# Kernel tuning notes

Measured on AMD Instinct MI355X. Metric: run time of the kernel, lower is better.

## Reference

```python
import jax, jax.numpy as jnp
import numpy as np

B, T, X, H, Z = 64, 2048, 128, 256, 64


def setup_inputs() -> dict:
    key = jax.random.key(0)
    ks = jax.random.split(key, 6)
    s = lambda n: 1.0 / np.sqrt(n).astype(np.float32)
    return {
        "x_seq": jax.random.normal(ks[0], (B, T, X), jnp.float32),
        # LSTMCell params packed as [i|f|g|o] gates. Flax: input dense has no bias,
        # hidden dense has bias.
        "Wi": jax.random.normal(ks[1], (X, 4 * H), jnp.float32) * s(X),
        "Wh": jax.random.normal(ks[2], (H, 4 * H), jnp.float32) * s(H),
        "bh": jnp.zeros((4 * H,), jnp.float32),
        # head: Dense(H) -> relu -> Dense(2Z)
        "W1": jax.random.normal(ks[3], (H, H), jnp.float32) * s(H),
        "b1": jnp.zeros((H,), jnp.float32),
        "W2": jax.random.normal(ks[4], (H, 2 * Z), jnp.float32) * s(H),
        "b2": jnp.zeros((2 * Z,), jnp.float32),
    }


def _forward(x_seq, Wi, Wh, bh, W1, b1, W2, b2):
    Bsz = x_seq.shape[0]
    Hd = Wh.shape[0]
    # Precompute input projection for all timesteps (one big GEMM).
    x_proj = jnp.einsum('btx,xg->btg', x_seq, Wi)  # (B, T, 4H)
    xp = jnp.swapaxes(x_proj, 0, 1)  # (T, B, 4H) for scan

    def step(carry, xp_t):
        c, h = carry
        gates = xp_t + h @ Wh + bh  # (B, 4H)
        i, f, g, o = jnp.split(gates, 4, axis=-1)
        i = jax.nn.sigmoid(i)
        f = jax.nn.sigmoid(f)
        g = jnp.tanh(g)
        o = jax.nn.sigmoid(o)
        c = f * c + i * g
        h = o * jnp.tanh(c)
        hid = jax.nn.relu(h @ W1 + b1)
        out = hid @ W2 + b2  # (B, 2Z)
        return (c, h), out

    c0 = jnp.zeros((Bsz, Hd), x_seq.dtype)
    h0 = jnp.zeros((Bsz, Hd), x_seq.dtype)
    _, outs = jax.lax.scan(step, (c0, h0), xp)  # outs: (T, B, 2Z)
    outs = jnp.swapaxes(outs, 0, 1)  # (B, T, 2Z)
    mu_seq, log_sigma_seq = jnp.split(outs, 2, axis=-1)
    return mu_seq, log_sigma_seq


def reference(x_seq, Wi, Wh, bh, W1, b1, W2, b2):
    return _forward(x_seq, Wi, Wh, bh, W1, b1, W2, b2)
```

## Files before the change

### kernel.cpp

```cpp
#include <hip/hip_runtime.h>

typedef _Float16 f16;
typedef _Float16 h2 __attribute__((ext_vector_type(2)));
typedef _Float16 h8 __attribute__((ext_vector_type(8)));
typedef float f4 __attribute__((ext_vector_type(4)));

constexpr int Bb = 64, Tt = 2048, Xx = 128, Hh = 256, G4 = 1024, Z2 = 128;

__device__ __forceinline__ float fdot2f(h2 a, h2 b, float c) {
#if __has_builtin(__builtin_amdgcn_fdot2)
  return __builtin_amdgcn_fdot2(a, b, c, false);
#else
  return c + (float)a[0] * (float)b[0] + (float)a[1] * (float)b[1];
#endif
}
__device__ __forceinline__ float tanhf_(float x) {
  float e = __expf(2.0f * x);
  return 1.0f - 2.0f * __builtin_amdgcn_rcpf(e + 1.0f);
}
__device__ __forceinline__ h2 bch2(unsigned int u) { return __builtin_bit_cast(h2, u); }

template <int CTRL>
__device__ __forceinline__ float qb(float v) {
  return __builtin_bit_cast(float,
      __builtin_amdgcn_mov_dpp(__builtin_bit_cast(int, v), CTRL, 0xf, 0xf, true));
}

__global__ void cast_f16_k(const float* __restrict__ in, f16* __restrict__ out, int n) {
  int i = (blockIdx.x * 256 + threadIdx.x) * 4;
  if (i >= n) return;
  float4 v = *(const float4*)(in + i);
  h2 a = {(f16)v.x, (f16)v.y};
  h2 b = {(f16)v.z, (f16)v.w};
  uint2 o = {__builtin_bit_cast(unsigned int, a), __builtin_bit_cast(unsigned int, b)};
  *(uint2*)(out + i) = o;
}

__global__ void cast_whT_k(const float* __restrict__ Wh, f16* __restrict__ WhT) {
  int idx = blockIdx.x * 256 + threadIdx.x;
  int r = idx >> 8, k = idx & 255;
  int gcol = ((r & 3) << 8) | (r >> 2);
  WhT[idx] = (f16)Wh[(long)k * G4 + gcol];
}

__global__ __launch_bounds__(256, 4) void gemm_f16_k(
    const f16* __restrict__ A, const f16* __restrict__ Bm, const float* __restrict__ bias,
    f16* __restrict__ C16, float* __restrict__ Cmu, float* __restrict__ Cls,
    int N, int K, int a_shift, int a_ostride, int a_t0,
    int mode, int o_t0, int tcshift)
{
  __shared__ __align__(16) f16 At[64][48];
  __shared__ __align__(16) f16 Bt[64][48];
  const int tid = threadIdx.x;
  const int mblk = blockIdx.x, nblk = blockIdx.y;
  const int w = tid >> 6, lane = tid & 63;

  const int sa_row = tid >> 2, sa_k = (tid & 3) * 8;
  const int m_g = mblk * 64 + sa_row;
  const long arow = (long)(m_g >> a_shift) * a_ostride + a_t0 + (m_g & ((1 << a_shift) - 1));
  const f16* aptr = A + arow * K + sa_k;
  const int sb_k = tid >> 3, sb_n = (tid & 7) * 8;
  const f16* bptr = Bm + (long)sb_k * N + nblk * 64 + sb_n;

  f4 acc[4];
#pragma unroll
  for (int i = 0; i < 4; ++i) acc[i] = (f4){0.f, 0.f, 0.f, 0.f};

  const int arow_l = w * 16 + (lane & 15);
  const int k0 = (lane >> 4) * 8;

  for (int kk = 0; kk < K; kk += 32) {
    uint4 av = *(const uint4*)(aptr + kk);
    uint4 bv = *(const uint4*)(bptr + (long)kk * N);
    __syncthreads();
    *(uint4*)&At[sa_row][sa_k] = av;
    h8 bx = __builtin_bit_cast(h8, bv);
#pragma unroll
    for (int j = 0; j < 8; ++j) Bt[sb_n + j][sb_k] = bx[j];
    __syncthreads();
    h8 af = *(const h8*)&At[arow_l][k0];
#pragma unroll
    for (int nt = 0; nt < 4; ++nt) {
      h8 bf = *(const h8*)&Bt[nt * 16 + (lane & 15)][k0];
      acc[nt] = __builtin_amdgcn_mfma_f32_16x16x32_f16(af, bf, acc[nt], 0, 0, 0);
    }
  }

  const int row_l = w * 16 + ((lane >> 4) << 2);
  const int col_l = lane & 15;
#pragma unroll
  for (int nt = 0; nt < 4; ++nt) {
    int gcol = nblk * 64 + nt * 16 + col_l;
    float bv = bias[gcol];
#pragma unroll
    for (int r = 0; r < 4; ++r) {
      int gm = mblk * 64 + row_l + r;
      float val = acc[nt][r] + bv;
      if (mode == 1) val = fmaxf(val, 0.f);
      if (mode <= 1) {
        C16[(long)gm * N + gcol] = (f16)val;
      } else {
        int bb = gm >> tcshift, tl = gm & ((1 << tcshift) - 1);
        long orow = (long)bb * Tt + o_t0 + tl;
        if (gcol < 64) Cmu[orow * 64 + gcol] = val;
        else Cls[orow * 64 + (gcol - 64)] = val;
      }
    }
  }
}

__global__ void __launch_bounds__(1024) __attribute__((amdgpu_waves_per_eu(4, 4)))
lstm_rec_k(
    const f16* __restrict__ WhT, const f16* __restrict__ xp,
    f16* __restrict__ hout, float* __restrict__ c_state, f16* __restrict__ h_state,
    int TC, int first)
{
  const int b = blockIdx.x, tid = threadIdx.x;
  const int j = tid >> 2, g = tid & 3;
  __shared__ __align__(16) h2 hbuf[2][128];
  __shared__ __align__(16) h2 wlds[9][1024][4];

  h2 w[92];
  {
    const uint4* p4 = (const uint4*)(WhT + (long)tid * Hh);
#pragma unroll
    for (int i = 0; i < 23; ++i) {
      uint4 v = p4[i];
      w[4 * i + 0] = bch2(v.x); w[4 * i + 1] = bch2(v.y);
      w[4 * i + 2] = bch2(v.z); w[4 * i + 3] = bch2(v.w);
    }
#pragma unroll
    for (int gg = 0; gg < 9; ++gg) *(uint4*)&wlds[gg][tid][0] = p4[23 + gg];
  }

  float c = first ? 0.f : c_state[b * Hh + j];
  if (tid < 128) {
    h2 hz = {(f16)0.f, (f16)0.f};
    hbuf[0][tid] = first ? hz : ((const h2*)h_state)[b * 128 + tid];
  }
  __syncthreads();

  const float sgn = (g == 2) ? 2.0f : -1.0f;
  const int xcol = (g << 8) | j;
  const f16* xptr = xp + (long)b * TC * G4 + xcol;
  const f16* xend = xptr + (long)(TC - 1) * G4;
  f16 xc = *xptr;
  int p = 0;
  for (int t = 0; t < TC; ++t) {
    const f16* xnp = (xptr == xend) ? xptr : xptr + G4;
    f16 xn = *xnp;

    float a0 = (float)xc, a1 = 0.f;
    const uint4* hb4 = (const uint4*)&hbuf[p][0];
#pragma unroll
    for (int i = 0; i < 23; ++i) {
      uint4 hv = hb4[i];
      a0 = fdot2f(w[4 * i + 0], bch2(hv.x), a0);
      a1 = fdot2f(w[4 * i + 1], bch2(hv.y), a1);
      a0 = fdot2f(w[4 * i + 2], bch2(hv.z), a0);
      a1 = fdot2f(w[4 * i + 3], bch2(hv.w), a1);
    }
#pragma unroll
    for (int gg = 0; gg < 9; ++gg) {
      uint4 hv = hb4[23 + gg];
      uint4 wv = *(const uint4*)&wlds[gg][tid][0];
      a0 = fdot2f(bch2(wv.x), bch2(hv.x), a0);
      a1 = fdot2f(bch2(wv.y), bch2(hv.y), a1);
      a0 = fdot2f(bch2(wv.z), bch2(hv.z), a0);
      a1 = fdot2f(bch2(wv.w), bch2(hv.w), a1);
    }
    float a = a0 + a1;

    float e = __expf(sgn * a);
    float r = __builtin_amdgcn_rcpf(1.0f + e);
    float act = (g == 2) ? 1.0f - 2.0f * r : r;

    float ai = qb<0x00>(act), af = qb<0x55>(act);
    float ag = qb<0xAA>(act), ao = qb<0xFF>(act);
    c = af * c + ai * ag;
    float hval = ao * tanhf_(c);
    if (g == 3) {
      f16 hh = (f16)hval;
      ((f16*)&hbuf[p ^ 1][0])[j] = hh;
      hout[((long)b * TC + t) * Hh + j] = hh;
    }
    __syncthreads();
    p ^= 1;
    xc = xn;
    xptr = xnp;
  }
  if (g == 0) c_state[b * Hh + j] = c;
  if (tid < 128) ((h2*)h_state)[b * 128 + tid] = hbuf[p][tid];
}

extern "C" void kernel_launch(void* const* d_in, const int* in_sizes, int n_in,
                              void* d_out, int out_size, void* d_ws, size_t ws_size,
                              hipStream_t stream)
{
  const float* x  = (const float*)d_in[0];
  const float* Wi = (const float*)d_in[1];
  const float* Wh = (const float*)d_in[2];
  const float* bh = (const float*)d_in[3];
  const float* W1 = (const float*)d_in[4];
  const float* b1 = (const float*)d_in[5];
  const float* W2 = (const float*)d_in[6];
  const float* b2 = (const float*)d_in[7];
  float* out = (float*)d_out;

  char* ws = (char*)d_ws;
  size_t off = 0;
  auto alloc = [&](size_t bytes) -> char* {
    char* p = ws + off;
    off = (off + bytes + 255) & ~(size_t)255;
    return p;
  };
  f16* x16   = (f16*)alloc((size_t)Bb * Tt * Xx * 2);
  f16* wi16  = (f16*)alloc((size_t)Xx * G4 * 2);
  f16* whT16 = (f16*)alloc((size_t)G4 * Hh * 2);
  f16* w116  = (f16*)alloc((size_t)Hh * Hh * 2);
  f16* w216  = (f16*)alloc((size_t)Hh * Z2 * 2);
  float* cst = (float*)alloc((size_t)Bb * Hh * 4);
  f16* hst   = (f16*)alloc((size_t)Bb * Hh * 2);

  int tc = 2048;
  while (tc > 32) {
    size_t need = (size_t)Bb * tc * G4 * 2 + (size_t)Bb * tc * Hh * 2;
    if (off + need <= ws_size) break;
    tc >>= 1;
  }
  int tcsh = __builtin_ctz((unsigned)tc);
  f16* xp16 = (f16*)alloc((size_t)Bb * tc * G4 * 2);
  f16* h16  = (f16*)alloc((size_t)Bb * tc * Hh * 2);
  f16* hid16 = xp16;

  cast_f16_k<<<(Bb * Tt * Xx) / 1024, 256, 0, stream>>>(x, x16, Bb * Tt * Xx);
  cast_f16_k<<<(Xx * G4) / 1024, 256, 0, stream>>>(Wi, wi16, Xx * G4);
  cast_f16_k<<<(Hh * Hh) / 1024, 256, 0, stream>>>(W1, w116, Hh * Hh);
  cast_f16_k<<<(Hh * Z2) / 1024, 256, 0, stream>>>(W2, w216, Hh * Z2);
  cast_whT_k<<<(Hh * G4) / 256, 256, 0, stream>>>(Wh, whT16);

  float* mu = out;
  float* ls = out + (size_t)Bb * Tt * 64;

  for (int t0 = 0; t0 < Tt; t0 += tc) {
    dim3 gx(Bb * tc / 64, G4 / 64);
    gemm_f16_k<<<gx, 256, 0, stream>>>(x16, wi16, bh, xp16, nullptr, nullptr,
                                       G4, Xx, tcsh, Tt, t0, 0, 0, 0);
    lstm_rec_k<<<Bb, 1024, 0, stream>>>(whT16, xp16, h16, cst, hst, tc, (t0 == 0) ? 1 : 0);
    dim3 g1g(Bb * tc / 64, Hh / 64);
    gemm_f16_k<<<g1g, 256, 0, stream>>>(h16, w116, b1, hid16, nullptr, nullptr,
                                        Hh, Hh, 30, 0, 0, 1, 0, 0);
    dim3 g2g(Bb * tc / 64, Z2 / 64);
    gemm_f16_k<<<g2g, 256, 0, stream>>>(hid16, w216, b2, nullptr, mu, ls,
                                        Z2, Hh, 30, 0, 0, 2, t0, tcsh);
  }
}
```

Measured before the change: 3.687 ms.

## Split LSTM recurrence K-dimension across quad lanes with DPP reduction

Repartitions the recurrent matvec so each lane of a 4-thread quad handles a 64-wide slice of the hidden vector for all four gates of unit j, instead of the full 256-wide dot product for one gate. Partial sums are combined with DPP quad reductions and each lane selects its gate's sum. Each lane now reads only its own 64-entry slice of h from LDS (plus padding against bank conflicts) rather than the whole 256 entries, cutting LDS read traffic per step. The weight transpose kernel is reindexed to match. The cost is extra cross-lane reduction instructions and more selection logic.

```diff
diff --git a/kernel.cpp b/kernel.cpp
--- a/kernel.cpp
+++ b/kernel.cpp
@@ -24,6 +24,11 @@
 __device__ __forceinline__ float qb(float v) {
   return __builtin_bit_cast(float,
       __builtin_amdgcn_mov_dpp(__builtin_bit_cast(int, v), CTRL, 0xf, 0xf, true));
+}
+__device__ __forceinline__ float qsum(float v) {
+  v += qb<0xB1>(v);
+  v += qb<0x4E>(v);
+  return v;
 }
 
 __global__ void cast_f16_k(const float* __restrict__ in, f16* __restrict__ out, int n) {
@@ -38,9 +43,12 @@
 
 __global__ void cast_whT_k(const float* __restrict__ Wh, f16* __restrict__ WhT) {
   int idx = blockIdx.x * 256 + threadIdx.x;
-  int r = idx >> 8, k = idx & 255;
-  int gcol = ((r & 3) << 8) | (r >> 2);
-  WhT[idx] = (f16)Wh[(long)k * G4 + gcol];
+  int tid = idx >> 8, r = idx & 255;
+  int s = r >> 1, e = r & 1;
+  int half = s >> 6, gate = (s >> 4) & 3, kk = s & 15;
+  int j = tid >> 2, q = tid & 3;
+  int k = q * 64 + half * 32 + kk * 2 + e;
+  WhT[idx] = (f16)Wh[(long)k * G4 + gate * 256 + j];
 }
 
 __global__ __launch_bounds__(256, 4) void gemm_f16_k(
@@ -109,20 +117,20 @@
   }
 }
 
-__global__ void __launch_bounds__(1024) __attribute__((amdgpu_waves_per_eu(4, 4)))
-lstm_rec_k(
+__attribute__((amdgpu_flat_work_group_size(1024, 1024), amdgpu_waves_per_eu(4, 4)))
+__global__ void lstm_rec_k(
     const f16* __restrict__ WhT, const f16* __restrict__ xp,
     f16* __restrict__ hout, float* __restrict__ c_state, f16* __restrict__ h_state,
     int TC, int first)
 {
   const int b = blockIdx.x, tid = threadIdx.x;
-  const int j = tid >> 2, g = tid & 3;
-  __shared__ __align__(16) h2 hbuf[2][128];
+  const int j = tid >> 2, q = tid & 3;
+  __shared__ __align__(16) h2 hbuf[2][4][36];
   __shared__ __align__(16) h2 wlds[9][1024][4];
 
   h2 w[92];
   {
-    const uint4* p4 = (const uint4*)(WhT + (long)tid * Hh);
+    const uint4* p4 = (const uint4*)(WhT + (long)tid * 256);
 #pragma unroll
     for (int i = 0; i < 23; ++i) {
       uint4 v = p4[i];
@@ -136,12 +144,12 @@
   float c = first ? 0.f : c_state[b * Hh + j];
   if (tid < 128) {
     h2 hz = {(f16)0.f, (f16)0.f};
-    hbuf[0][tid] = first ? hz : ((const h2*)h_state)[b * 128 + tid];
+    hbuf[0][tid >> 5][tid & 31] = first ? hz : ((const h2*)h_state)[b * 128 + tid];
   }
   __syncthreads();
 
-  const float sgn = (g == 2) ? 2.0f : -1.0f;
-  const int xcol = (g << 8) | j;
+  const float sgn = (q == 2) ? 2.0f : -1.0f;
+  const int xcol = (q << 8) | j;
   const f16* xptr = xp + (long)b * TC * G4 + xcol;
   const f16* xend = xptr + (long)(TC - 1) * G4;
   f16 xc = *xptr;
@@ -150,38 +158,76 @@
     const f16* xnp = (xptr == xend) ? xptr : xptr + G4;
     f16 xn = *xnp;
 
-    float a0 = (float)xc, a1 = 0.f;
-    const uint4* hb4 = (const uint4*)&hbuf[p][0];
-#pragma unroll
-    for (int i = 0; i < 23; ++i) {
-      uint4 hv = hb4[i];
-      a0 = fdot2f(w[4 * i + 0], bch2(hv.x), a0);
-      a1 = fdot2f(w[4 * i + 1], bch2(hv.y), a1);
-      a0 = fdot2f(w[4 * i + 2], bch2(hv.z), a0);
-      a1 = fdot2f(w[4 * i + 3], bch2(hv.w), a1);
-    }
-#pragma unroll
-    for (int gg = 0; gg < 9; ++gg) {
-      uint4 hv = hb4[23 + gg];
-      uint4 wv = *(const uint4*)&wlds[gg][tid][0];
-      a0 = fdot2f(bch2(wv.x), bch2(hv.x), a0);
-      a1 = fdot2f(bch2(wv.y), bch2(hv.y), a1);
-      a0 = fdot2f(bch2(wv.z), bch2(hv.z), a0);
-      a1 = fdot2f(bch2(wv.w), bch2(hv.w), a1);
-    }
-    float a = a0 + a1;
+    const uint4* hq = (const uint4*)&hbuf[p][q][0];
+    float d0 = 0.f, d1 = 0.f, d2 = 0.f, d3 = 0.f;
+    {
+      uint4 ha = hq[0], hb_ = hq[1], hc = hq[2], hd = hq[3];
+      h2 hh0[16] = {bch2(ha.x),  bch2(ha.y),  bch2(ha.z),  bch2(ha.w),
+                    bch2(hb_.x), bch2(hb_.y), bch2(hb_.z), bch2(hb_.w),
+                    bch2(hc.x),  bch2(hc.y),  bch2(hc.z),  bch2(hc.w),
+                    bch2(hd.x),  bch2(hd.y),  bch2(hd.z),  bch2(hd.w)};
+#pragma unroll
+      for (int m = 0; m < 16; ++m) {
+        d0 = fdot2f(w[m], hh0[m], d0);
+        d1 = fdot2f(w[16 + m], hh0[m], d1);
+        d2 = fdot2f(w[32 + m], hh0[m], d2);
+        d3 = fdot2f(w[48 + m], hh0[m], d3);
+      }
+    }
+    {
+      uint4 ha = hq[4], hb_ = hq[5], hc = hq[6], hd = hq[7];
+      h2 hh1[16] = {bch2(ha.x),  bch2(ha.y),  bch2(ha.z),  bch2(ha.w),
+                    bch2(hb_.x), bch2(hb_.y), bch2(hb_.z), bch2(hb_.w),
+                    bch2(hc.x),  bch2(hc.y),  bch2(hc.z),  bch2(hc.w),
+                    bch2(hd.x),  bch2(hd.y),  bch2(hd.z),  bch2(hd.w)};
+#pragma unroll
+      for (int m = 0; m < 16; ++m) d0 = fdot2f(w[64 + m], hh1[m], d0);
+#pragma unroll
+      for (int m = 0; m < 12; ++m) d1 = fdot2f(w[80 + m], hh1[m], d1);
+      {
+        uint4 wv = *(const uint4*)&wlds[0][tid][0];
+        d1 = fdot2f(bch2(wv.x), hh1[12], d1);
+        d1 = fdot2f(bch2(wv.y), hh1[13], d1);
+        d1 = fdot2f(bch2(wv.z), hh1[14], d1);
+        d1 = fdot2f(bch2(wv.w), hh1[15], d1);
+      }
+#pragma unroll
+      for (int gg = 1; gg <= 4; ++gg) {
+        uint4 wv = *(const uint4*)&wlds[gg][tid][0];
+        int m0 = 4 * (gg - 1);
+        d2 = fdot2f(bch2(wv.x), hh1[m0 + 0], d2);
+        d2 = fdot2f(bch2(wv.y), hh1[m0 + 1], d2);
+        d2 = fdot2f(bch2(wv.z), hh1[m0 + 2], d2);
+        d2 = fdot2f(bch2(wv.w), hh1[m0 + 3], d2);
+      }
+#pragma unroll
+      for (int gg = 5; gg <= 8; ++gg) {
+        uint4 wv = *(const uint4*)&wlds[gg][tid][0];
+        int m0 = 4 * (gg - 5);
+        d3 = fdot2f(bch2(wv.x), hh1[m0 + 0], d3);
+        d3 = fdot2f(bch2(wv.y), hh1[m0 + 1], d3);
+        d3 = fdot2f(bch2(wv.z), hh1[m0 + 2], d3);
+        d3 = fdot2f(bch2(wv.w), hh1[m0 + 3], d3);
+      }
+    }
+
+    d0 = qsum(d0); d1 = qsum(d1); d2 = qsum(d2); d3 = qsum(d3);
+    float a = (q & 1) ? d1 : d0;
+    float b2_ = (q & 1) ? d3 : d2;
+    a = (q & 2) ? b2_ : a;
+    a += (float)xc;
 
     float e = __expf(sgn * a);
     float r = __builtin_amdgcn_rcpf(1.0f + e);
-    float act = (g == 2) ? 1.0f - 2.0f * r : r;
+    float act = (q == 2) ? 1.0f - 2.0f * r : r;
 
     float ai = qb<0x00>(act), af = qb<0x55>(act);
     float ag = qb<0xAA>(act), ao = qb<0xFF>(act);
     c = af * c + ai * ag;
     float hval = ao * tanhf_(c);
-    if (g == 3) {
+    if (q == 3) {
       f16 hh = (f16)hval;
-      ((f16*)&hbuf[p ^ 1][0])[j] = hh;
+      ((f16*)&hbuf[p ^ 1][0][0])[(j >> 6) * 72 + (j & 63)] = hh;
       hout[((long)b * TC + t) * Hh + j] = hh;
     }
     __syncthreads();
@@ -189,8 +235,8 @@
     xc = xn;
     xptr = xnp;
   }
-  if (g == 0) c_state[b * Hh + j] = c;
-  if (tid < 128) ((h2*)h_state)[b * 128 + tid] = hbuf[p][tid];
+  if (q == 0) c_state[b * Hh + j] = c;
+  if (tid < 128) ((h2*)h_state)[b * 128 + tid] = hbuf[p][tid >> 5][tid & 31];
 }
 
 extern "C" void kernel_launch(void* const* d_in, const int* in_sizes, int n_in,
```

Result: faster. 3.567 ms (-3.3%).
